# Kernel optimization log

Measured on AMD Instinct MI355X. Metric: run time of the kernel, lower is better.

## Reference

```python
import jax, jax.numpy as jnp
import numpy as np

B, L1, L2, DIN, H, DK, DV = 16, 1024, 1024, 1024, 16, 64, 64


def setup_inputs() -> dict:
    key = jax.random.key(0)
    ks = jax.random.split(key, 9)
    s = 1.0 / np.sqrt(DIN)
    return {
        "x": jax.random.normal(ks[0], (B, L1, DIN), dtype=jnp.float32),
        "y": jax.random.normal(ks[1], (B, L2, DIN), dtype=jnp.float32),
        "y_mask": jax.random.randint(ks[2], (B, L2), 0, 2) == 1,  # True => masked
        "Wq": jax.random.normal(ks[3], (DIN, H * DK), dtype=jnp.float32) * s,
        "bq": jnp.zeros((H * DK,), dtype=jnp.float32),
        "Wk": jax.random.normal(ks[4], (DIN, H * DK), dtype=jnp.float32) * s,
        "bk": jnp.zeros((H * DK,), dtype=jnp.float32),
        "Wv": jax.random.normal(ks[5], (DIN, H * DV), dtype=jnp.float32) * s,
        "bv": jnp.zeros((H * DV,), dtype=jnp.float32),
    }


def reference(x, y, y_mask, Wq, bq, Wk, bk, Wv, bv):
    b, l1, _ = x.shape
    l2 = y.shape[1]
    # QKV projections, split into heads: [b, len, H, d]
    q = (x @ Wq + bq).reshape(b, l1, H, DK)
    k = (y @ Wk + bk).reshape(b, l2, H, DK)
    v = (y @ Wv + bv).reshape(b, l2, H, DV)
    # (do_relu=False -> no relu)
    scores = jnp.einsum("bqhd,bkhd->bhqk", q, k) / jnp.sqrt(jnp.float32(DK))
    scores = jnp.where(y_mask[:, None, None, :], -jnp.inf, scores)
    alpha = jax.nn.softmax(scores, axis=-1)  # over len2
    out = jnp.einsum("bhqk,bkhd->bqhd", alpha, v)
    return out.reshape(b, l1, H * DV)
```

## Files before the change

kernel.cpp:

```cpp
#include <hip/hip_runtime.h>
#include <hip/hip_bf16.h>

#define BATCH 16
#define L1D 1024
#define L2D 1024
#define DIN 1024
#define NH 16
#define HD 1024
#define OHD 3072

typedef __attribute__((ext_vector_type(4))) float floatx4;
typedef __attribute__((ext_vector_type(8))) short shortx8;
typedef __attribute__((ext_vector_type(8))) unsigned short ushortx8;

#if __has_builtin(__builtin_amdgcn_exp2f)
#define EXP2(x) __builtin_amdgcn_exp2f(x)
#else
#define EXP2(x) exp2f(x)
#endif

static __device__ __forceinline__ unsigned short f2bf(float f) {
    union { float f; unsigned u; } v; v.f = f;
    unsigned r = v.u + 0x7fff + ((v.u >> 16) & 1);
    return (unsigned short)(r >> 16);
}
static __device__ __forceinline__ unsigned short f2bf_fast(float f) {
    union { float f; unsigned u; } v; v.f = f;
    return (unsigned short)((v.u + 0x8000u) >> 16);
}

#define GLOBAL_AS __attribute__((address_space(1)))
#define LDS_AS __attribute__((address_space(3)))
static __device__ __forceinline__ void gl2lds16(const unsigned short* g, unsigned short* l) {
    __builtin_amdgcn_global_load_lds((const GLOBAL_AS unsigned int*)g,
                                     (LDS_AS unsigned int*)l, 16, 0, 0);
}

#define CFENCE() asm volatile("" ::: "memory")

#define NCVT 8192
__global__ void prep_kernel(const float* __restrict__ x, const float* __restrict__ y,
                            unsigned short* __restrict__ xb, unsigned short* __restrict__ yb,
                            const int* __restrict__ ym, float* __restrict__ biasf) {
    int bid = blockIdx.x;
    if (bid < 2 * NCVT) {
        const float* in = bid < NCVT ? x : y;
        unsigned short* o = bid < NCVT ? xb : yb;
        int bb = bid < NCVT ? bid : bid - NCVT;
        size_t i = ((size_t)bb * 256 + threadIdx.x) * 8;
        float4 a = *(const float4*)(in + i);
        float4 b = *(const float4*)(in + i + 4);
        ushortx8 v;
        v[0] = f2bf(a.x); v[1] = f2bf(a.y); v[2] = f2bf(a.z); v[3] = f2bf(a.w);
        v[4] = f2bf(b.x); v[5] = f2bf(b.y); v[6] = f2bf(b.z); v[7] = f2bf(b.w);
        *(ushortx8*)(o + i) = v;
    } else {
        int i = (bid - 2 * NCVT) * 256 + threadIdx.x;
        biasf[i] = ym[i] ? -INFINITY : 0.0f;
    }
}

__global__ void wt_kernel(const float* __restrict__ Wq, const float* __restrict__ Wk,
                          const float* __restrict__ Wv, unsigned short* __restrict__ Wt) {
    __shared__ float tile[32][33];
    const float* W = blockIdx.z == 0 ? Wq : (blockIdx.z == 1 ? Wk : Wv);
    unsigned short* dst = Wt + (size_t)blockIdx.z * HD * DIN;
    int bx = blockIdx.x, by = blockIdx.y;
    int tx = threadIdx.x, ty = threadIdx.y;
    for (int i = 0; i < 4; i++)
        tile[ty + i * 8][tx] = W[(size_t)(by * 32 + ty + i * 8) * HD + bx * 32 + tx];
    __syncthreads();
    for (int i = 0; i < 4; i++)
        dst[(size_t)(bx * 32 + ty + i * 8) * DIN + by * 32 + tx] = f2bf(tile[tx][ty + i * 8]);
}

__global__ __launch_bounds__(512, 2) void gemm_kernel(
    const unsigned short* __restrict__ xb, const unsigned short* __restrict__ yb,
    const unsigned short* __restrict__ Wt,
    const float* __restrict__ bq, const float* __restrict__ bk, const float* __restrict__ bvp,
    unsigned short* __restrict__ Out, float qscale)
{
    __shared__ unsigned short As[2][256 * 64];
    __shared__ unsigned short Bs[2][256 * 64];

    int f = blockIdx.y * gridDim.x + blockIdx.x;
    int swz = (f & 7) * 96 + (f >> 3);
    const int n0 = (swz % 12) * 256;
    const int m0 = (swz / 12) * 256;
    const int sec = n0 >> 10;
    const unsigned short* Aptr = (sec == 0) ? xb : yb;
    const float* bias = (sec == 0) ? bq : (sec == 1 ? bk : bvp);
    const float scale = (sec == 0) ? qscale : 1.0f;

    const int tid = threadIdx.x;
    const int wid = tid >> 6, lane = tid & 63;
    const int c = lane & 15, qd = lane >> 4;
    const int cswz = c & 7;
    const int R0 = (wid >> 2) * 128;
    const int C0 = (wid & 3) * 64;

    const int srow = tid >> 3;
    const int sphys = tid & 7;
    const int scol = (sphys ^ (srow & 7)) * 8;

    floatx4 acc[8][4] = {};
    shortx8 a[4][2];
    shortx8 b0[2][2], b1[2][2];

    auto dsrdA = [&](int mq, const unsigned short* buf) {
#pragma unroll
        for (int i = 0; i < 4; i++)
#pragma unroll
            for (int kk = 0; kk < 2; kk++)
                a[i][kk] = *(const shortx8*)&buf[(R0 + mq * 64 + i * 16 + c) * 64 +
                                                 (((kk * 4 + qd) ^ cswz) * 8)];
    };
    auto dsrdB = [&](shortx8 (&bt)[2][2], int nq, const unsigned short* buf) {
#pragma unroll
        for (int j = 0; j < 2; j++)
#pragma unroll
            for (int kk = 0; kk < 2; kk++)
                bt[j][kk] = *(const shortx8*)&buf[(C0 + (nq * 2 + j) * 16 + c) * 64 +
                                                  (((kk * 4 + qd) ^ cswz) * 8)];
    };
    auto mfmaQ = [&](int mq, int nq, shortx8 (&bt)[2][2]) {
        __builtin_amdgcn_s_setprio(1);
#pragma unroll
        for (int kk = 0; kk < 2; kk++)
#pragma unroll
            for (int i = 0; i < 4; i++)
#pragma unroll
                for (int j = 0; j < 2; j++)
                    acc[mq * 4 + i][nq * 2 + j] = __builtin_amdgcn_mfma_f32_16x16x32_bf16(
                        a[i][kk], bt[j][kk], acc[mq * 4 + i][nq * 2 + j], 0, 0, 0);
        __builtin_amdgcn_s_setprio(0);
    };
    auto stageA = [&](unsigned short* dst, int h, int kt) {
        const unsigned short* g = Aptr + (size_t)(m0 + h * 128 + srow) * DIN + kt * 64 + scol;
        unsigned short* l = dst + (h * 128 + srow) * 64 + sphys * 8;
        gl2lds16(g, l);
        gl2lds16(g + (size_t)64 * DIN, l + 64 * 64);
    };
    auto stageB = [&](unsigned short* dst, int h, int kt) {
        const unsigned short* g = Wt + (size_t)(n0 + h * 128 + srow) * DIN + kt * 64 + scol;
        unsigned short* l = dst + (h * 128 + srow) * 64 + sphys * 8;
        gl2lds16(g, l);
        gl2lds16(g + (size_t)64 * DIN, l + 64 * 64);
    };

    float biasv[4];
#pragma unroll
    for (int nf = 0; nf < 4; nf++)
        biasv[nf] = bias[((n0 & 1023) + C0 + nf * 16 + c) & 1023];
    asm volatile("s_waitcnt vmcnt(0)" ::: "memory");

    stageB(Bs[0], 0, 0); stageB(Bs[0], 1, 0);
    stageA(As[0], 0, 0); stageA(As[0], 1, 0);
    stageB(Bs[1], 0, 1); stageB(Bs[1], 1, 1);
    asm volatile("s_waitcnt vmcnt(4)" ::: "memory");
    CFENCE(); __builtin_amdgcn_s_barrier(); CFENCE();

    for (int it = 0; it < 8; ++it) {
        const int kt1 = 2 * it + 1;
        const int ktp = 2 * it + 2;
        const bool pf = (it < 7);

        dsrdA(0, As[0]); dsrdB(b0, 0, Bs[0]);
        stageA(As[1], 0, kt1);
        CFENCE(); __builtin_amdgcn_s_barrier(); CFENCE();
        mfmaQ(0, 0, b0);
        CFENCE(); __builtin_amdgcn_s_barrier(); CFENCE();

        dsrdB(b1, 1, Bs[0]);
        stageA(As[1], 1, kt1);
        CFENCE(); __builtin_amdgcn_s_barrier(); CFENCE();
        mfmaQ(0, 1, b1);
        CFENCE(); __builtin_amdgcn_s_barrier(); CFENCE();

        dsrdA(1, As[0]);
        if (pf) stageB(Bs[0], 0, ktp);
        CFENCE(); __builtin_amdgcn_s_barrier(); CFENCE();
        mfmaQ(1, 1, b1);
        CFENCE(); __builtin_amdgcn_s_barrier(); CFENCE();

        if (pf) stageB(Bs[0], 1, ktp);
        CFENCE(); __builtin_amdgcn_s_barrier(); CFENCE();
        mfmaQ(1, 0, b0);
        if (pf) asm volatile("s_waitcnt vmcnt(4)" ::: "memory");
        else    asm volatile("s_waitcnt vmcnt(0)" ::: "memory");
        CFENCE(); __builtin_amdgcn_s_barrier(); CFENCE();

        dsrdA(0, As[1]); dsrdB(b0, 0, Bs[1]);
        if (pf) stageA(As[0], 0, ktp);
        CFENCE(); __builtin_amdgcn_s_barrier(); CFENCE();
        mfmaQ(0, 0, b0);
        CFENCE(); __builtin_amdgcn_s_barrier(); CFENCE();

        dsrdB(b1, 1, Bs[1]);
        if (pf) stageA(As[0], 1, ktp);
        CFENCE(); __builtin_amdgcn_s_barrier(); CFENCE();
        mfmaQ(0, 1, b1);
        CFENCE(); __builtin_amdgcn_s_barrier(); CFENCE();

        dsrdA(1, As[1]);
        if (pf) stageB(Bs[1], 0, ktp + 1);
        CFENCE(); __builtin_amdgcn_s_barrier(); CFENCE();
        mfmaQ(1, 1, b1);
        CFENCE(); __builtin_amdgcn_s_barrier(); CFENCE();

        if (pf) stageB(Bs[1], 1, ktp + 1);
        CFENCE(); __builtin_amdgcn_s_barrier(); CFENCE();
        mfmaQ(1, 0, b0);
        if (pf) asm volatile("s_waitcnt vmcnt(4)" ::: "memory");
        CFENCE(); __builtin_amdgcn_s_barrier(); CFENCE();
    }

    unsigned short* reg0 = (wid < 4) ? (&As[0][0] + wid * 8192)
                                     : (&Bs[0][0] + (wid - 4) * 8192);
#pragma unroll
    for (int mf = 0; mf < 8; mf++)
#pragma unroll
        for (int r = 0; r < 4; r++) {
            const int lrow = mf * 16 + qd * 4 + r;
#pragma unroll
            for (int nf = 0; nf < 4; nf++) {
                const int lcol = (nf * 16 + c) ^ (qd * 16);
                reg0[lrow * 64 + lcol] = f2bf((acc[mf][nf][r] + biasv[nf]) * scale);
            }
        }
    __syncthreads();
#pragma unroll
    for (int p = 0; p < 16; p++) {
        const int gr = p * 16 + (tid >> 5);
        const int gc8 = (tid & 31) * 8;
        const int wr = ((gr >> 7) << 2) + (gc8 >> 6);
        const unsigned short* rg = (wr < 4) ? (&As[0][0] + wr * 8192)
                                            : (&Bs[0][0] + (wr - 4) * 8192);
        const int lrow = gr & 127;
        const int lcol = (gc8 & 63) ^ (((lrow >> 2) & 3) * 16);
        ushortx8 vv = *(const ushortx8*)&rg[lrow * 64 + lcol];
        *(ushortx8*)(Out + (size_t)(m0 + gr) * OHD + n0 + gc8) = vv;
    }
}

__global__ void vt_kernel(const unsigned short* __restrict__ V,
                          unsigned short* __restrict__ Vt) {
    __shared__ unsigned short t[64][72];
    const int l20 = blockIdx.x * 64;
    const int bh  = blockIdx.y;
    const int b = bh >> 4, h = bh & 15;
    const int tid = threadIdx.x;
    for (int i = 0; i < 2; i++) {
        int idx = i * 256 + tid;
        int row = idx >> 3, col = (idx & 7) * 8;
        *(ushortx8*)(&t[row][col]) =
            *(const ushortx8*)(V + (size_t)(b * L2D + l20 + row) * OHD + h * 64 + col);
    }
    __syncthreads();
    for (int i = 0; i < 2; i++) {
        int idx = i * 256 + tid;
        int dv = idx >> 3, col = (idx & 7) * 8;
        ushortx8 v;
        for (int j = 0; j < 8; j++) v[j] = t[col + j][dv];
        *(ushortx8*)(Vt + (size_t)(bh * 64 + dv) * L2D + l20 + col) = v;
    }
}

__global__ __launch_bounds__(256, 4) void attn_kernel(
    const unsigned short* __restrict__ QK,
    const unsigned short* __restrict__ Vt, const float* __restrict__ biasf,
    float* __restrict__ out)
{
    __shared__ unsigned short Ks[64 * 64];
    __shared__ unsigned short Vs[64 * 64];
    __shared__ unsigned short Ps[4][32 * 72];

    int f = blockIdx.y * gridDim.x + blockIdx.x;
    int bh = (f & 7) * 32 + (f >> 6);
    int q0 = ((f >> 3) & 7) * 128;
    const int b = bh >> 4, h = bh & 15;
    const int tid = threadIdx.x, wid = tid >> 6, lane = tid & 63;
    const int c = lane & 15, qd = lane >> 4;

    shortx8 qf[2][2];
    for (int mt2 = 0; mt2 < 2; mt2++)
        for (int kt = 0; kt < 2; kt++)
            qf[mt2][kt] = *(const shortx8*)(QK +
                (size_t)(b * L1D + q0 + wid * 32 + mt2 * 16 + c) * OHD + h * 64 + kt * 32 + qd * 8);

    floatx4 o[2][4] = {};
    float psum[2][4] = {};

    const unsigned short* Kbase = QK + HD + (size_t)b * L2D * OHD + h * 64;
    const unsigned short* Vbase = Vt + (size_t)bh * 64 * L2D;
    const float* bb = biasf + b * L2D;

    int idxa = tid, idxb = 256 + tid;
    int rowa = idxa >> 3, sca = ((idxa & 7) ^ (rowa & 7)) * 8;
    int rowb = idxb >> 3, scb = ((idxb & 7) ^ (rowb & 7)) * 8;
    const int swz8 = c & 7;

    for (int kv0 = 0; kv0 < L2D; kv0 += 64) {
        gl2lds16(Kbase + (size_t)(kv0 + rowa) * OHD + sca, &Ks[idxa * 8]);
        gl2lds16(Vbase + (size_t)rowa * L2D + kv0 + sca, &Vs[idxa * 8]);
        gl2lds16(Kbase + (size_t)(kv0 + rowb) * OHD + scb, &Ks[idxb * 8]);
        gl2lds16(Vbase + (size_t)rowb * L2D + kv0 + scb, &Vs[idxb * 8]);
        __syncthreads();

        float bv[4];
        for (int nt = 0; nt < 4; nt++) bv[nt] = bb[kv0 + nt * 16 + c];

        for (int mt2 = 0; mt2 < 2; mt2++) {
            for (int nt = 0; nt < 4; nt++) {
                floatx4 z = {};
                for (int kt = 0; kt < 2; kt++) {
                    shortx8 kf = *(shortx8*)(&Ks[(nt * 16 + c) * 64 + ((kt * 4 + qd) ^ swz8) * 8]);
                    z = __builtin_amdgcn_mfma_f32_16x16x32_bf16(qf[mt2][kt], kf, z, 0, 0, 0);
                }
                for (int r = 0; r < 4; r++) {
                    float p = EXP2(z[r] + bv[nt]);
                    psum[mt2][r] += p;
                    Ps[wid][(mt2 * 16 + qd * 4 + r) * 72 + nt * 16 + c] = f2bf_fast(p);
                }
            }
        }
        for (int mt2 = 0; mt2 < 2; mt2++) {
            shortx8 pf[2];
            for (int kt = 0; kt < 2; kt++)
                pf[kt] = *(shortx8*)(&Ps[wid][(mt2 * 16 + c) * 72 + kt * 32 + qd * 8]);
            for (int nt = 0; nt < 4; nt++)
                for (int kt = 0; kt < 2; kt++) {
                    shortx8 vf = *(shortx8*)(&Vs[(nt * 16 + c) * 64 + ((kt * 4 + qd) ^ swz8) * 8]);
                    o[mt2][nt] = __builtin_amdgcn_mfma_f32_16x16x32_bf16(pf[kt], vf, o[mt2][nt], 0, 0, 0);
                }
        }
        __syncthreads();
    }

    for (int mt2 = 0; mt2 < 2; mt2++)
        for (int r = 0; r < 4; r++) {
            float l = psum[mt2][r];
            for (int off = 1; off < 16; off <<= 1)
                l += __shfl_xor(l, off, 64);
            float inv = 1.0f / l;
            size_t rowbase = ((size_t)b * L1D + q0 + wid * 32 + mt2 * 16 + qd * 4 + r) * HD + h * 64;
            for (int nt = 0; nt < 4; nt++)
                out[rowbase + nt * 16 + c] = o[mt2][nt][r] * inv;
        }
}

extern "C" void kernel_launch(void* const* d_in, const int* in_sizes, int n_in,
                              void* d_out, int out_size, void* d_ws, size_t ws_size,
                              hipStream_t stream) {
    const float* x  = (const float*)d_in[0];
    const float* y  = (const float*)d_in[1];
    const int*  ym  = (const int*)d_in[2];
    const float* Wq = (const float*)d_in[3];
    const float* bq = (const float*)d_in[4];
    const float* Wk = (const float*)d_in[5];
    const float* bk = (const float*)d_in[6];
    const float* Wv = (const float*)d_in[7];
    const float* bv = (const float*)d_in[8];
    float* outp = (float*)d_out;

    const size_t M = (size_t)BATCH * L1D;
    const size_t T = M * HD;
    unsigned short* Obuf = (unsigned short*)d_ws;
    unsigned short* xb   = Obuf + M * OHD;
    unsigned short* yb   = xb + T;
    unsigned short* Wt   = yb + T;
    float* biasf         = (float*)(Wt + (size_t)OHD * DIN);

    const float QSCALE = 0.125f * 1.44269504088896340736f;

    prep_kernel<<<2 * NCVT + (BATCH * L2D) / 256, 256, 0, stream>>>(x, y, xb, yb, ym, biasf);
    wt_kernel<<<dim3(HD / 32, DIN / 32, 3), dim3(32, 8), 0, stream>>>(Wq, Wk, Wv, Wt);
    gemm_kernel<<<dim3(OHD / 256, M / 256), 512, 0, stream>>>(xb, yb, Wt, bq, bk, bv, Obuf, QSCALE);
    vt_kernel<<<dim3(L2D / 64, BATCH * NH), 256, 0, stream>>>(Obuf + 2 * HD, xb);
    attn_kernel<<<dim3(L1D / 128, BATCH * NH), 256, 0, stream>>>(Obuf, xb, biasf, outp);
}
```

Before: 398.3 us.

## Load K and V fragments directly from global memory instead of staging in LDS

Removes the shared-memory staging of K and V tiles and the block-wide barriers around them. Each wave now reads its MFMA operand fragments for K and V straight from global memory, relying on L1/L2 caches to serve the reuse across the four waves and the two query subtiles. Loop pragmas for full unrolling are added as well. This cuts LDS traffic and synchronisation, but each K/V element is now fetched redundantly by every wave, which adds global/cache load pressure and latency with no explicit prefetch.

```diff
diff --git a/kernel.cpp b/kernel.cpp
--- a/kernel.cpp
+++ b/kernel.cpp
@@ -271,8 +271,6 @@
     const unsigned short* __restrict__ Vt, const float* __restrict__ biasf,
     float* __restrict__ out)
 {
-    __shared__ unsigned short Ks[64 * 64];
-    __shared__ unsigned short Vs[64 * 64];
     __shared__ unsigned short Ps[4][32 * 72];
 
     int f = blockIdx.y * gridDim.x + blockIdx.x;
@@ -291,32 +289,27 @@
     floatx4 o[2][4] = {};
     float psum[2][4] = {};
 
-    const unsigned short* Kbase = QK + HD + (size_t)b * L2D * OHD + h * 64;
-    const unsigned short* Vbase = Vt + (size_t)bh * 64 * L2D;
+    const unsigned short* Kb = QK + HD + (size_t)b * L2D * OHD + h * 64 + qd * 8;
+    const unsigned short* Vb = Vt + (size_t)bh * 64 * L2D + qd * 8;
     const float* bb = biasf + b * L2D;
 
-    int idxa = tid, idxb = 256 + tid;
-    int rowa = idxa >> 3, sca = ((idxa & 7) ^ (rowa & 7)) * 8;
-    int rowb = idxb >> 3, scb = ((idxb & 7) ^ (rowb & 7)) * 8;
-    const int swz8 = c & 7;
-
     for (int kv0 = 0; kv0 < L2D; kv0 += 64) {
-        gl2lds16(Kbase + (size_t)(kv0 + rowa) * OHD + sca, &Ks[idxa * 8]);
-        gl2lds16(Vbase + (size_t)rowa * L2D + kv0 + sca, &Vs[idxa * 8]);
-        gl2lds16(Kbase + (size_t)(kv0 + rowb) * OHD + scb, &Ks[idxb * 8]);
-        gl2lds16(Vbase + (size_t)rowb * L2D + kv0 + scb, &Vs[idxb * 8]);
-        __syncthreads();
-
         float bv[4];
+#pragma unroll
         for (int nt = 0; nt < 4; nt++) bv[nt] = bb[kv0 + nt * 16 + c];
 
+#pragma unroll
         for (int mt2 = 0; mt2 < 2; mt2++) {
+#pragma unroll
             for (int nt = 0; nt < 4; nt++) {
                 floatx4 z = {};
+#pragma unroll
                 for (int kt = 0; kt < 2; kt++) {
-                    shortx8 kf = *(shortx8*)(&Ks[(nt * 16 + c) * 64 + ((kt * 4 + qd) ^ swz8) * 8]);
+                    shortx8 kf = *(const shortx8*)(Kb +
+                        (size_t)(kv0 + nt * 16 + c) * OHD + kt * 32);
                     z = __builtin_amdgcn_mfma_f32_16x16x32_bf16(qf[mt2][kt], kf, z, 0, 0, 0);
                 }
+#pragma unroll
                 for (int r = 0; r < 4; r++) {
                     float p = EXP2(z[r] + bv[nt]);
                     psum[mt2][r] += p;
@@ -324,17 +317,21 @@
                 }
             }
         }
+#pragma unroll
         for (int mt2 = 0; mt2 < 2; mt2++) {
             shortx8 pf[2];
+#pragma unroll
             for (int kt = 0; kt < 2; kt++)
                 pf[kt] = *(shortx8*)(&Ps[wid][(mt2 * 16 + c) * 72 + kt * 32 + qd * 8]);
+#pragma unroll
             for (int nt = 0; nt < 4; nt++)
+#pragma unroll
                 for (int kt = 0; kt < 2; kt++) {
-                    shortx8 vf = *(shortx8*)(&Vs[(nt * 16 + c) * 64 + ((kt * 4 + qd) ^ swz8) * 8]);
+                    shortx8 vf = *(const shortx8*)(Vb +
+                        (size_t)(nt * 16 + c) * L2D + kv0 + kt * 32);
                     o[mt2][nt] = __builtin_amdgcn_mfma_f32_16x16x32_bf16(pf[kt], vf, o[mt2][nt], 0, 0, 0);
                 }
         }
-        __syncthreads();
     }
 
     for (int mt2 = 0; mt2 < 2; mt2++)
```

Measured after the change: 635.5 us. +59.6%, slower.
